# Optimization experiments

Measured on AMD Instinct MI355X. Metric: run time of the kernel, lower is better.

The kernel has to match this reference:

```python
import jax, jax.numpy as jnp
import numpy as np

R_ITER = 3
EPS = 1e-7  # keras.backend.epsilon()


def squash(v, axis=-1):
    s2 = jnp.sum(jnp.square(v), axis=axis, keepdims=True)
    scale = s2 / (1.0 + s2) / jnp.sqrt(s2 + EPS)
    return scale * v


def setup_inputs() -> dict:
    key = jax.random.key(0)
    kx, kw = jax.random.split(key)
    B, N_IN, D_IN = 64, 2048, 8
    N_OUT, D_OUT = 32, 16
    x = jax.random.normal(kx, (B, N_IN, D_IN), dtype=jnp.float32)
    # W matches keras weight (1, N_IN//shared, N_OUT, D_OUT, D_IN) with shared=1,
    # stored here without the leading broadcast dim. RandomNormal(stddev=0.1).
    W = 0.1 * jax.random.normal(kw, (N_IN, N_OUT, D_OUT, D_IN), dtype=jnp.float32)
    return {"x": x, "W": W}


def reference(x, W):
    # predictions u_hat[b, i, j, :] = W[i, j] @ x[b, i]  -> [B, N_in, N_out, D_out]
    preds = jnp.einsum('nodi,bni->bnod', W, x)
    N_in, N_out = preds.shape[1], preds.shape[2]
    # raw routing logits start at zeros with broadcast batch dim (as in TF code)
    raw = jnp.zeros((1, N_in, N_out), dtype=x.dtype)
    for i in range(R_ITER):
        rw = jax.nn.softmax(raw, axis=2)                      # softmax over output caps
        s = jnp.sum(rw[..., None] * preds, axis=1)            # [B, N_out, D_out]
        v = squash(s, axis=-1)                                # squash over capsule dim
        if i < R_ITER - 1:
            # agreement: <u_hat_ij, v_j>
            raw = raw + jnp.einsum('bnod,bod->bno', preds, v)
    return v, rw
```

## Files before the change

### kernel.cpp

```cpp
#include <hip/hip_runtime.h>

static constexpr int B_    = 64;
static constexpr int N_    = 2048;
static constexpr int DI_   = 8;
static constexpr int O_    = 32;
static constexpr int P_    = 16;
static constexpr int OP_   = O_ * P_;
static constexpr int M_    = OP_ * B_;
static constexpr int CHUNK_ = 8;
static constexpr int NBLK_  = N_ / CHUNK_;

template <int MODE, bool ATOMIC>
__global__ __launch_bounds__(1024, 4)
void fused_pass(const float* __restrict__ x, const float* __restrict__ W,
                const float* __restrict__ v_in, float* __restrict__ s_out,
                float* __restrict__ rw_out) {
  __shared__ float x_lds[CHUNK_ * 8 * 65];
  __shared__ float a_lds[2][O_ * B_];
  const int tid  = threadIdx.x;
  const int lane = tid & 63;
  const int wave = tid >> 6;
  const int n0   = blockIdx.x * CHUNK_;

  #pragma unroll
  for (int k = 0; k < 4; ++k) {
    int d = k * 1024 + tid;
    int b = d >> 6, rem = d & 63;
    x_lds[rem * 65 + b] = x[b * (N_ * DI_) + n0 * DI_ + rem];
  }

  float s_r[32];
  #pragma unroll
  for (int q = 0; q < 32; ++q) s_r[q] = 0.0f;

  __syncthreads();

  #pragma unroll 1
  for (int nn = 0; nn < CHUNK_; ++nn) {
    const int n = n0 + nn;
    float xr[8];
    #pragma unroll
    for (int i = 0; i < 8; ++i) xr[i] = x_lds[(nn * 8 + i) * 65 + lane];

    float pr[2][16];
    float ao0 = 0.0f, ao1 = 0.0f;

    #pragma unroll
    for (int oo = 0; oo < 2; ++oo) {
      const int o_u = __builtin_amdgcn_readfirstlane(wave * 2 + oo);
      const float* wp = W + (size_t)(n * O_ + o_u) * (P_ * DI_);

      float4 va0, va1, va2, va3;
      if (MODE != 0) {
        const float4* vp =
            (const float4*)(v_in + (size_t)lane * OP_ + (wave * 2 + oo) * P_);
        va0 = vp[0]; va1 = vp[1]; va2 = vp[2]; va3 = vp[3];
      }

      float acc = 0.0f;
      #pragma unroll
      for (int p = 0; p < P_; ++p) {
        float pv = wp[p * 8 + 0] * xr[0];
        pv = __builtin_fmaf(wp[p * 8 + 1], xr[1], pv);
        pv = __builtin_fmaf(wp[p * 8 + 2], xr[2], pv);
        pv = __builtin_fmaf(wp[p * 8 + 3], xr[3], pv);
        pv = __builtin_fmaf(wp[p * 8 + 4], xr[4], pv);
        pv = __builtin_fmaf(wp[p * 8 + 5], xr[5], pv);
        pv = __builtin_fmaf(wp[p * 8 + 6], xr[6], pv);
        pv = __builtin_fmaf(wp[p * 8 + 7], xr[7], pv);
        if (MODE == 0) {
          s_r[oo * 16 + p] += pv;
        } else {
          pr[oo][p] = pv;
          const float vc = (p < 4)  ? ((p & 3) == 0 ? va0.x : (p & 3) == 1 ? va0.y : (p & 3) == 2 ? va0.z : va0.w)
                         : (p < 8)  ? ((p & 3) == 0 ? va1.x : (p & 3) == 1 ? va1.y : (p & 3) == 2 ? va1.z : va1.w)
                         : (p < 12) ? ((p & 3) == 0 ? va2.x : (p & 3) == 1 ? va2.y : (p & 3) == 2 ? va2.z : va2.w)
                                    : ((p & 3) == 0 ? va3.x : (p & 3) == 1 ? va3.y : (p & 3) == 2 ? va3.z : va3.w);
          acc = __builtin_fmaf(pv, vc, acc);
        }
      }
      if (MODE != 0) {
        if (oo == 0) ao0 = acc; else ao1 = acc;
        a_lds[nn & 1][(wave * 2 + oo) * B_ + lane] = acc;
      }
    }

    if (MODE != 0) {
      __syncthreads();

      float Z = 0.0f;
      #pragma unroll
      for (int o = 0; o < O_; ++o) Z += __expf(a_lds[nn & 1][o * B_ + lane]);
      const float rZ  = 1.0f / Z;
      const float rw0 = __expf(ao0) * rZ;
      const float rw1 = __expf(ao1) * rZ;

      #pragma unroll
      for (int p = 0; p < P_; ++p) {
        s_r[p]      = __builtin_fmaf(rw0, pr[0][p], s_r[p]);
        s_r[16 + p] = __builtin_fmaf(rw1, pr[1][p], s_r[16 + p]);
      }
      if (MODE == 2) {
        float2 t; t.x = rw0; t.y = rw1;
        *(float2*)(rw_out + ((size_t)lane * N_ + n) * O_ + wave * 2) = t;
      }
    }
  }

  if (ATOMIC) {
    #pragma unroll
    for (int oo = 0; oo < 2; ++oo) {
      float* sp = s_out + (size_t)((wave * 2 + oo) * P_) * B_ + lane;
      #pragma unroll
      for (int p = 0; p < P_; ++p) atomicAdd(&sp[p * B_], s_r[oo * 16 + p]);
    }
  } else {
    #pragma unroll
    for (int oo = 0; oo < 2; ++oo) {
      float* sp = s_out + (size_t)blockIdx.x * M_ +
                  (size_t)((wave * 2 + oo) * P_) * B_ + lane;
      #pragma unroll
      for (int p = 0; p < P_; ++p) sp[p * B_] = s_r[oo * 16 + p];
    }
  }
}

__global__ __launch_bounds__(1024)
void reduce1(const float* __restrict__ spart, float* __restrict__ p2, int K) {
  const int g  = blockIdx.x >> 4;
  const int mc = blockIdx.x & 15;
  const int kpg = K >> 4;
  const int m0 = mc * 2048 + threadIdx.x;
  float a0 = 0.0f, a1 = 0.0f;
  const float* p = spart + (size_t)(g * kpg) * M_;
  for (int k = 0; k < kpg; ++k) {
    a0 += p[(size_t)k * M_ + m0];
    a1 += p[(size_t)k * M_ + m0 + 1024];
  }
  p2[(size_t)g * M_ + m0]        = a0;
  p2[(size_t)g * M_ + m0 + 1024] = a1;
}

__global__ __launch_bounds__(1024)
void v_kernel(const float* __restrict__ src, int ngroups, float scale,
              const float* __restrict__ v_add, float* __restrict__ v_out,
              float* __restrict__ zero_buf) {
  __shared__ float sq[P_ * 64];
  const int t = threadIdx.x;
  const int b = t & 63;
  const int p = t >> 6;
  const int o = blockIdx.x;
  const int q = o * P_ + p;
  float acc = 0.0f;
  for (int g = 0; g < ngroups; ++g) acc += src[(size_t)g * M_ + q * 64 + b];
  acc *= scale;
  sq[p * 64 + b] = acc * acc;
  if (zero_buf) zero_buf[blockIdx.x * 1024 + t] = 0.0f;
  __syncthreads();
  float s2 = 0.0f;
  #pragma unroll
  for (int pp = 0; pp < P_; ++pp) s2 += sq[pp * 64 + b];
  float sc = (s2 / (1.0f + s2)) / sqrtf(s2 + 1e-7f);
  float v = acc * sc;
  const int idx = b * OP_ + q;
  v_out[idx] = v + (v_add ? v_add[idx] : 0.0f);
}

extern "C" void kernel_launch(void* const* d_in, const int* in_sizes, int n_in,
                              void* d_out, int out_size, void* d_ws, size_t ws_size,
                              hipStream_t stream) {
  (void)in_sizes; (void)n_in; (void)out_size;
  const float* x = (const float*)d_in[0];
  const float* W = (const float*)d_in[1];
  float* out_v  = (float*)d_out;
  float* out_rw = out_v + (size_t)B_ * O_ * P_;
  float* vws   = (float*)d_ws;
  float* vsum  = vws + M_;
  float* p2    = vsum + M_;
  float* spart = p2 + 16 * M_;

  const size_t need = (size_t)(2 * M_ + 16 * M_ + (size_t)NBLK_ * M_) * 4;

  dim3 gF(NBLK_), bF(1024), gV(O_), bV(1024), gR(256);
  if (ws_size >= need) {
    fused_pass<0, false><<<gF, bF, 0, stream>>>(x, W, nullptr, spart, nullptr);
    reduce1<<<gR, bF, 0, stream>>>(spart, p2, NBLK_);
    v_kernel<<<gV, bV, 0, stream>>>(p2, 16, 1.0f / 32.0f, nullptr, vws, nullptr);
    fused_pass<1, false><<<gF, bF, 0, stream>>>(x, W, vws, spart, nullptr);
    reduce1<<<gR, bF, 0, stream>>>(spart, p2, NBLK_);
    v_kernel<<<gV, bV, 0, stream>>>(p2, 16, 1.0f, vws, vsum, nullptr);
    fused_pass<2, false><<<gF, bF, 0, stream>>>(x, W, vsum, spart, out_rw);
    reduce1<<<gR, bF, 0, stream>>>(spart, p2, NBLK_);
    v_kernel<<<gV, bV, 0, stream>>>(p2, 16, 1.0f, nullptr, out_v, nullptr);
  } else {
    float* sAb = p2;
    float* sBb = sAb + M_;
    hipMemsetAsync(sAb, 0, (size_t)M_ * sizeof(float), stream);
    fused_pass<0, true><<<gF, bF, 0, stream>>>(x, W, nullptr, sAb, nullptr);
    v_kernel<<<gV, bV, 0, stream>>>(sAb, 1, 1.0f / 32.0f, nullptr, vws, sBb);
    fused_pass<1, true><<<gF, bF, 0, stream>>>(x, W, vws, sBb, nullptr);
    v_kernel<<<gV, bV, 0, stream>>>(sBb, 1, 1.0f, vws, vsum, sAb);
    fused_pass<2, true><<<gF, bF, 0, stream>>>(x, W, vsum, sAb, out_rw);
    v_kernel<<<gV, bV, 0, stream>>>(sAb, 1, 1.0f, nullptr, out_v, nullptr);
  }
}
```

Measured before the change: 271.5 us.

## Double-buffer W slices into LDS via async global_load_lds and cut softmax exps

Each wave now streams its 1 KB portion of the next capsule's W slice straight into a double-buffered LDS array with global_load_lds, waiting on vmcnt before use. The FMA loop then reads W as float4 from LDS instead of issuing per-element global (scalar) loads. The v vectors are loaded once per block into registers rather than on every capsule. The softmax normaliser is built from per-wave partial sums of exponentials, so each thread does two expf plus 16 LDS adds instead of 32 expf. The larger LDS footprint may reduce how many blocks fit per CU, and the hand-written waitcnt relies on vmcnt ordering.

```diff
diff --git a/kernel.cpp b/kernel.cpp
--- a/kernel.cpp
+++ b/kernel.cpp
@@ -9,6 +9,14 @@
 static constexpr int M_    = OP_ * B_;
 static constexpr int CHUNK_ = 8;
 static constexpr int NBLK_  = N_ / CHUNK_;
+static constexpr int WSLICE_ = O_ * P_ * DI_;
+
+__device__ __forceinline__ void stage_w16(const float* g, float* l) {
+  __builtin_amdgcn_global_load_lds(
+      (const __attribute__((address_space(1))) void*)g,
+      (__attribute__((address_space(3))) void*)l,
+      16, 0, 0);
+}
 
 template <int MODE, bool ATOMIC>
 __global__ __launch_bounds__(1024, 4)
@@ -16,7 +24,8 @@
                 const float* __restrict__ v_in, float* __restrict__ s_out,
                 float* __restrict__ rw_out) {
   __shared__ float x_lds[CHUNK_ * 8 * 65];
-  __shared__ float a_lds[2][O_ * B_];
+  __shared__ __align__(16) float w_lds[2][WSLICE_];
+  __shared__ float z_lds[2][16 * B_];
   const int tid  = threadIdx.x;
   const int lane = tid & 63;
   const int wave = tid >> 6;
@@ -29,15 +38,41 @@
     x_lds[rem * 65 + b] = x[b * (N_ * DI_) + n0 * DI_ + rem];
   }
 
+  float va[2][16];
+  if (MODE != 0) {
+    #pragma unroll
+    for (int oo = 0; oo < 2; ++oo) {
+      const float4* vp =
+          (const float4*)(v_in + (size_t)lane * OP_ + (wave * 2 + oo) * P_);
+      const float4 t0 = vp[0], t1 = vp[1], t2 = vp[2], t3 = vp[3];
+      va[oo][0]  = t0.x; va[oo][1]  = t0.y; va[oo][2]  = t0.z; va[oo][3]  = t0.w;
+      va[oo][4]  = t1.x; va[oo][5]  = t1.y; va[oo][6]  = t1.z; va[oo][7]  = t1.w;
+      va[oo][8]  = t2.x; va[oo][9]  = t2.y; va[oo][10] = t2.z; va[oo][11] = t2.w;
+      va[oo][12] = t3.x; va[oo][13] = t3.y; va[oo][14] = t3.z; va[oo][15] = t3.w;
+    }
+  }
+
   float s_r[32];
   #pragma unroll
   for (int q = 0; q < 32; ++q) s_r[q] = 0.0f;
 
+  stage_w16(W + (size_t)n0 * WSLICE_ + wave * 256 + lane * 4,
+            &w_lds[0][wave * 256]);
+
   __syncthreads();
 
   #pragma unroll 1
   for (int nn = 0; nn < CHUNK_; ++nn) {
     const int n = n0 + nn;
+
+    if (nn + 1 < CHUNK_) {
+      stage_w16(W + (size_t)(n + 1) * WSLICE_ + wave * 256 + lane * 4,
+                &w_lds[(nn + 1) & 1][wave * 256]);
+      asm volatile("s_waitcnt vmcnt(1)" ::: "memory");
+    } else {
+      asm volatile("s_waitcnt vmcnt(0)" ::: "memory");
+    }
+
     float xr[8];
     #pragma unroll
     for (int i = 0; i < 8; ++i) xr[i] = x_lds[(nn * 8 + i) * 65 + lane];
@@ -47,53 +82,42 @@
 
     #pragma unroll
     for (int oo = 0; oo < 2; ++oo) {
-      const int o_u = __builtin_amdgcn_readfirstlane(wave * 2 + oo);
-      const float* wp = W + (size_t)(n * O_ + o_u) * (P_ * DI_);
-
-      float4 va0, va1, va2, va3;
-      if (MODE != 0) {
-        const float4* vp =
-            (const float4*)(v_in + (size_t)lane * OP_ + (wave * 2 + oo) * P_);
-        va0 = vp[0]; va1 = vp[1]; va2 = vp[2]; va3 = vp[3];
-      }
-
+      const float4* wl = (const float4*)&w_lds[nn & 1][(wave * 2 + oo) * 128];
       float acc = 0.0f;
       #pragma unroll
       for (int p = 0; p < P_; ++p) {
-        float pv = wp[p * 8 + 0] * xr[0];
-        pv = __builtin_fmaf(wp[p * 8 + 1], xr[1], pv);
-        pv = __builtin_fmaf(wp[p * 8 + 2], xr[2], pv);
-        pv = __builtin_fmaf(wp[p * 8 + 3], xr[3], pv);
-        pv = __builtin_fmaf(wp[p * 8 + 4], xr[4], pv);
-        pv = __builtin_fmaf(wp[p * 8 + 5], xr[5], pv);
-        pv = __builtin_fmaf(wp[p * 8 + 6], xr[6], pv);
-        pv = __builtin_fmaf(wp[p * 8 + 7], xr[7], pv);
+        const float4 w0 = wl[2 * p];
+        const float4 w1 = wl[2 * p + 1];
+        float pv = w0.x * xr[0];
+        pv = __builtin_fmaf(w0.y, xr[1], pv);
+        pv = __builtin_fmaf(w0.z, xr[2], pv);
+        pv = __builtin_fmaf(w0.w, xr[3], pv);
+        pv = __builtin_fmaf(w1.x, xr[4], pv);
+        pv = __builtin_fmaf(w1.y, xr[5], pv);
+        pv = __builtin_fmaf(w1.z, xr[6], pv);
+        pv = __builtin_fmaf(w1.w, xr[7], pv);
         if (MODE == 0) {
           s_r[oo * 16 + p] += pv;
         } else {
           pr[oo][p] = pv;
-          const float vc = (p < 4)  ? ((p & 3) == 0 ? va0.x : (p & 3) == 1 ? va0.y : (p & 3) == 2 ? va0.z : va0.w)
-                         : (p < 8)  ? ((p & 3) == 0 ? va1.x : (p & 3) == 1 ? va1.y : (p & 3) == 2 ? va1.z : va1.w)
-                         : (p < 12) ? ((p & 3) == 0 ? va2.x : (p & 3) == 1 ? va2.y : (p & 3) == 2 ? va2.z : va2.w)
-                                    : ((p & 3) == 0 ? va3.x : (p & 3) == 1 ? va3.y : (p & 3) == 2 ? va3.z : va3.w);
-          acc = __builtin_fmaf(pv, vc, acc);
+          acc = __builtin_fmaf(pv, va[oo][p], acc);
         }
       }
-      if (MODE != 0) {
-        if (oo == 0) ao0 = acc; else ao1 = acc;
-        a_lds[nn & 1][(wave * 2 + oo) * B_ + lane] = acc;
-      }
+      if (MODE != 0) { if (oo == 0) ao0 = acc; else ao1 = acc; }
     }
 
     if (MODE != 0) {
+      const float e0 = __expf(ao0);
+      const float e1 = __expf(ao1);
+      z_lds[nn & 1][wave * B_ + lane] = e0 + e1;
       __syncthreads();
 
       float Z = 0.0f;
       #pragma unroll
-      for (int o = 0; o < O_; ++o) Z += __expf(a_lds[nn & 1][o * B_ + lane]);
+      for (int w = 0; w < 16; ++w) Z += z_lds[nn & 1][w * B_ + lane];
       const float rZ  = 1.0f / Z;
-      const float rw0 = __expf(ao0) * rZ;
-      const float rw1 = __expf(ao1) * rZ;
+      const float rw0 = e0 * rZ;
+      const float rw1 = e1 * rZ;
 
       #pragma unroll
       for (int p = 0; p < P_; ++p) {
```

Result: faster. 229.6 us (-15.4%).

## Remap fused pass to stage W slices in LDS and reduce softmax with DPP

Applied to the files above, without the earlier changes.

The fused routing pass now assigns lanes to (output capsule, half of pose vector) and waves to batch groups of four. Each W slice for the next input capsule is double-buffered into LDS with global_load_lds using an XOR swizzle, and x values are broadcast through readfirstlane. The per-row softmax over output capsules becomes a DPP/shuffle reduction instead of an LDS exchange plus barrier, and partial sums are written as float4 in b-major layout. The v_kernel is adjusted to that layout. This is meant to cut redundant global W reads and scattered stores, at the cost of a barrier per step and more register pressure.

```diff
diff --git a/kernel.cpp b/kernel.cpp
--- a/kernel.cpp
+++ b/kernel.cpp
@@ -9,118 +9,160 @@
 static constexpr int M_    = OP_ * B_;
 static constexpr int CHUNK_ = 8;
 static constexpr int NBLK_  = N_ / CHUNK_;
+static constexpr int WSLICE_ = O_ * P_ * DI_;
+
+__device__ __forceinline__ void stage_w16(const float* g, float* l) {
+  __builtin_amdgcn_global_load_lds(
+      (const __attribute__((address_space(1))) void*)g,
+      (__attribute__((address_space(3))) void*)l,
+      16, 0, 0);
+}
+
+template <int CTRL>
+__device__ __forceinline__ float dpp_add(float v) {
+  int t = __builtin_amdgcn_update_dpp(0, __float_as_int(v), CTRL, 0xf, 0xf, false);
+  return v + __int_as_float(t);
+}
+
+__device__ __forceinline__ float rfl(float v) {
+  return __int_as_float(__builtin_amdgcn_readfirstlane(__float_as_int(v)));
+}
 
 template <int MODE, bool ATOMIC>
 __global__ __launch_bounds__(1024, 4)
 void fused_pass(const float* __restrict__ x, const float* __restrict__ W,
                 const float* __restrict__ v_in, float* __restrict__ s_out,
                 float* __restrict__ rw_out) {
-  __shared__ float x_lds[CHUNK_ * 8 * 65];
-  __shared__ float a_lds[2][O_ * B_];
+  __shared__ __align__(16) float w_lds[2][WSLICE_];
+  __shared__ __align__(16) float x_lds[CHUNK_ * 512];
   const int tid  = threadIdx.x;
   const int lane = tid & 63;
   const int wave = tid >> 6;
+  const int wu   = __builtin_amdgcn_readfirstlane(wave);
+  const int o    = lane >> 1;
+  const int ph   = lane & 1;
+  const int q3   = o & 7;
   const int n0   = blockIdx.x * CHUNK_;
 
+  {
+    const int bs = tid >> 4;
+    const int cs = tid & 15;
+    const float4 xv =
+        *(const float4*)(x + (size_t)bs * (N_ * DI_) + n0 * DI_ + cs * 4);
+    *(float4*)&x_lds[(cs >> 1) * 512 + bs * 8 + (cs & 1) * 4] = xv;
+  }
+
+  float vv[4][8];
+  if (MODE != 0) {
+    #pragma unroll
+    for (int bb = 0; bb < 4; ++bb) {
+      const float4* vp = (const float4*)(v_in + (size_t)(wu * 4 + bb) * OP_ +
+                                         o * P_ + ph * 8);
+      const float4 a = vp[0], c = vp[1];
+      vv[bb][0] = a.x; vv[bb][1] = a.y; vv[bb][2] = a.z; vv[bb][3] = a.w;
+      vv[bb][4] = c.x; vv[bb][5] = c.y; vv[bb][6] = c.z; vv[bb][7] = c.w;
+    }
+  }
+
+  float s_r[4][8];
   #pragma unroll
-  for (int k = 0; k < 4; ++k) {
-    int d = k * 1024 + tid;
-    int b = d >> 6, rem = d & 63;
-    x_lds[rem * 65 + b] = x[b * (N_ * DI_) + n0 * DI_ + rem];
-  }
-
-  float s_r[32];
-  #pragma unroll
-  for (int q = 0; q < 32; ++q) s_r[q] = 0.0f;
-
-  __syncthreads();
+  for (int bb = 0; bb < 4; ++bb)
+    #pragma unroll
+    for (int pp = 0; pp < 8; ++pp) s_r[bb][pp] = 0.0f;
+
+  const int sg = tid ^ ((tid >> 5) & 7);
+
+  stage_w16(W + (size_t)n0 * WSLICE_ + (size_t)sg * 4, &w_lds[0][wu * 256]);
 
   #pragma unroll 1
   for (int nn = 0; nn < CHUNK_; ++nn) {
-    const int n = n0 + nn;
-    float xr[8];
-    #pragma unroll
-    for (int i = 0; i < 8; ++i) xr[i] = x_lds[(nn * 8 + i) * 65 + lane];
-
-    float pr[2][16];
-    float ao0 = 0.0f, ao1 = 0.0f;
-
-    #pragma unroll
-    for (int oo = 0; oo < 2; ++oo) {
-      const int o_u = __builtin_amdgcn_readfirstlane(wave * 2 + oo);
-      const float* wp = W + (size_t)(n * O_ + o_u) * (P_ * DI_);
-
-      float4 va0, va1, va2, va3;
-      if (MODE != 0) {
-        const float4* vp =
-            (const float4*)(v_in + (size_t)lane * OP_ + (wave * 2 + oo) * P_);
-        va0 = vp[0]; va1 = vp[1]; va2 = vp[2]; va3 = vp[3];
-      }
-
-      float acc = 0.0f;
+    asm volatile("s_waitcnt vmcnt(0)" ::: "memory");
+    __syncthreads();
+    if (nn + 1 < CHUNK_)
+      stage_w16(W + (size_t)(n0 + nn + 1) * WSLICE_ + (size_t)sg * 4,
+                &w_lds[(nn + 1) & 1][wu * 256]);
+
+    float xs[4][8];
+    #pragma unroll
+    for (int bb = 0; bb < 4; ++bb) {
+      const float4 xa = *(const float4*)&x_lds[nn * 512 + (wu * 4 + bb) * 8];
+      const float4 xc = *(const float4*)&x_lds[nn * 512 + (wu * 4 + bb) * 8 + 4];
+      xs[bb][0] = rfl(xa.x); xs[bb][1] = rfl(xa.y);
+      xs[bb][2] = rfl(xa.z); xs[bb][3] = rfl(xa.w);
+      xs[bb][4] = rfl(xc.x); xs[bb][5] = rfl(xc.y);
+      xs[bb][6] = rfl(xc.z); xs[bb][7] = rfl(xc.w);
+    }
+
+    float pr[4][8];
+    float acc[4] = {0.0f, 0.0f, 0.0f, 0.0f};
+    const int wbase = ((nn & 1) ? WSLICE_ : 0) + o * 128 + ph * 64;
+
+    #pragma unroll
+    for (int pp = 0; pp < 8; ++pp) {
+      const int c0 = (2 * pp) ^ q3;
+      const int c1 = (2 * pp + 1) ^ q3;
+      const float4 w0 = *(const float4*)&w_lds[0][wbase + c0 * 4];
+      const float4 w1 = *(const float4*)&w_lds[0][wbase + c1 * 4];
       #pragma unroll
-      for (int p = 0; p < P_; ++p) {
-        float pv = wp[p * 8 + 0] * xr[0];
-        pv = __builtin_fmaf(wp[p * 8 + 1], xr[1], pv);
-        pv = __builtin_fmaf(wp[p * 8 + 2], xr[2], pv);
-        pv = __builtin_fmaf(wp[p * 8 + 3], xr[3], pv);
-        pv = __builtin_fmaf(wp[p * 8 + 4], xr[4], pv);
-        pv = __builtin_fmaf(wp[p * 8 + 5], xr[5], pv);
-        pv = __builtin_fmaf(wp[p * 8 + 6], xr[6], pv);
-        pv = __builtin_fmaf(wp[p * 8 + 7], xr[7], pv);
+      for (int bb = 0; bb < 4; ++bb) {
+        float pv = w0.x * xs[bb][0];
+        pv = __builtin_fmaf(w0.y, xs[bb][1], pv);
+        pv = __builtin_fmaf(w0.z, xs[bb][2], pv);
+        pv = __builtin_fmaf(w0.w, xs[bb][3], pv);
+        pv = __builtin_fmaf(w1.x, xs[bb][4], pv);
+        pv = __builtin_fmaf(w1.y, xs[bb][5], pv);
+        pv = __builtin_fmaf(w1.z, xs[bb][6], pv);
+        pv = __builtin_fmaf(w1.w, xs[bb][7], pv);
         if (MODE == 0) {
-          s_r[oo * 16 + p] += pv;
+          s_r[bb][pp] += pv;
         } else {
-          pr[oo][p] = pv;
-          const float vc = (p < 4)  ? ((p & 3) == 0 ? va0.x : (p & 3) == 1 ? va0.y : (p & 3) == 2 ? va0.z : va0.w)
-                         : (p < 8)  ? ((p & 3) == 0 ? va1.x : (p & 3) == 1 ? va1.y : (p & 3) == 2 ? va1.z : va1.w)
-                         : (p < 12) ? ((p & 3) == 0 ? va2.x : (p & 3) == 1 ? va2.y : (p & 3) == 2 ? va2.z : va2.w)
-                                    : ((p & 3) == 0 ? va3.x : (p & 3) == 1 ? va3.y : (p & 3) == 2 ? va3.z : va3.w);
-          acc = __builtin_fmaf(pv, vc, acc);
+          pr[bb][pp] = pv;
+          acc[bb] = __builtin_fmaf(pv, vv[bb][pp], acc[bb]);
         }
       }
-      if (MODE != 0) {
-        if (oo == 0) ao0 = acc; else ao1 = acc;
-        a_lds[nn & 1][(wave * 2 + oo) * B_ + lane] = acc;
+    }
+
+    if (MODE != 0) {
+      #pragma unroll
+      for (int bb = 0; bb < 4; ++bb) {
+        const float full = dpp_add<0xB1>(acc[bb]);
+        const float e = __expf(full);
+        float srow = e;
+        srow = dpp_add<0x121>(srow);
+        srow = dpp_add<0x122>(srow);
+        srow = dpp_add<0x124>(srow);
+        srow = dpp_add<0x128>(srow);
+        float t2 = srow + __shfl_xor(srow, 16);
+        const float S = t2 + __shfl_xor(t2, 32);
+        const float rw = (2.0f * e) / S;
+        #pragma unroll
+        for (int pp = 0; pp < 8; ++pp)
+          s_r[bb][pp] = __builtin_fmaf(rw, pr[bb][pp], s_r[bb][pp]);
+        if (MODE == 2) {
+          if (ph == 0)
+            rw_out[((size_t)(wu * 4 + bb) * N_ + (n0 + nn)) * O_ + o] = rw;
+        }
       }
     }
-
-    if (MODE != 0) {
-      __syncthreads();
-
-      float Z = 0.0f;
+  }
+
+  if (ATOMIC) {
+    #pragma unroll
+    for (int bb = 0; bb < 4; ++bb) {
+      float* sp = s_out + (size_t)(wu * 4 + bb) * OP_ + o * P_ + ph * 8;
       #pragma unroll
-      for (int o = 0; o < O_; ++o) Z += __expf(a_lds[nn & 1][o * B_ + lane]);
-      const float rZ  = 1.0f / Z;
-      const float rw0 = __expf(ao0) * rZ;
-      const float rw1 = __expf(ao1) * rZ;
-
-      #pragma unroll
-      for (int p = 0; p < P_; ++p) {
-        s_r[p]      = __builtin_fmaf(rw0, pr[0][p], s_r[p]);
-        s_r[16 + p] = __builtin_fmaf(rw1, pr[1][p], s_r[16 + p]);
-      }
-      if (MODE == 2) {
-        float2 t; t.x = rw0; t.y = rw1;
-        *(float2*)(rw_out + ((size_t)lane * N_ + n) * O_ + wave * 2) = t;
-      }
-    }
-  }
-
-  if (ATOMIC) {
-    #pragma unroll
-    for (int oo = 0; oo < 2; ++oo) {
-      float* sp = s_out + (size_t)((wave * 2 + oo) * P_) * B_ + lane;
-      #pragma unroll
-      for (int p = 0; p < P_; ++p) atomicAdd(&sp[p * B_], s_r[oo * 16 + p]);
+      for (int pp = 0; pp < 8; ++pp) atomicAdd(&sp[pp], s_r[bb][pp]);
     }
   } else {
     #pragma unroll
-    for (int oo = 0; oo < 2; ++oo) {
+    for (int bb = 0; bb < 4; ++bb) {
       float* sp = s_out + (size_t)blockIdx.x * M_ +
-                  (size_t)((wave * 2 + oo) * P_) * B_ + lane;
-      #pragma unroll
-      for (int p = 0; p < P_; ++p) sp[p * B_] = s_r[oo * 16 + p];
+                  (size_t)(wu * 4 + bb) * OP_ + o * P_ + ph * 8;
+      float4 st0, st1;
+      st0.x = s_r[bb][0]; st0.y = s_r[bb][1]; st0.z = s_r[bb][2]; st0.w = s_r[bb][3];
+      st1.x = s_r[bb][4]; st1.y = s_r[bb][5]; st1.z = s_r[bb][6]; st1.w = s_r[bb][7];
+      *(float4*)sp = st0;
+      *(float4*)(sp + 4) = st1;
     }
   }
 }
@@ -145,21 +187,22 @@
 void v_kernel(const float* __restrict__ src, int ngroups, float scale,
               const float* __restrict__ v_add, float* __restrict__ v_out,
               float* __restrict__ zero_buf) {
-  __shared__ float sq[P_ * 64];
+  __shared__ float sq[P_ * 65];
   const int t = threadIdx.x;
-  const int b = t & 63;
-  const int p = t >> 6;
+  const int p = t & 15;
+  const int b = t >> 4;
   const int o = blockIdx.x;
   const int q = o * P_ + p;
   float acc = 0.0f;
-  for (int g = 0; g < ngroups; ++g) acc += src[(size_t)g * M_ + q * 64 + b];
+  for (int g = 0; g < ngroups; ++g)
+    acc += src[(size_t)g * M_ + (size_t)b * OP_ + q];
   acc *= scale;
-  sq[p * 64 + b] = acc * acc;
+  sq[p * 65 + b] = acc * acc;
   if (zero_buf) zero_buf[blockIdx.x * 1024 + t] = 0.0f;
   __syncthreads();
   float s2 = 0.0f;
   #pragma unroll
-  for (int pp = 0; pp < P_; ++pp) s2 += sq[pp * 64 + b];
+  for (int pp = 0; pp < P_; ++pp) s2 += sq[pp * 65 + b];
   float sc = (s2 / (1.0f + s2)) / sqrtf(s2 + 1e-7f);
   float v = acc * sc;
   const int idx = b * OP_ + q;
```

After: 272.4 us. Within noise of the previous version (+0.4%).

## Compute capsule predictions with split-bf16 MFMA and batch-split blocks

Applied to the files above, without the earlier changes.

Replaces the scalar FP32 FMA prediction loop with 16x16x32 bf16 MFMA instructions, using a hi/lo bf16 split (three MFMAs) to approximate FP32 precision. Each block now covers half the batch with 512 threads, and agreement dot-products are reduced with cross-lane shuffles. The s-partial layout changes to batch-major, written through an LDS transpose epilogue, and v_kernel is remapped to match. The MFMA uses only K=8 of its 32 slots and the split conversion adds ALU work, so the gain over FP32 FMA depends on the kernel being compute-bound rather than memory-bound.

```diff
diff --git a/kernel.cpp b/kernel.cpp
--- a/kernel.cpp
+++ b/kernel.cpp
@@ -1,4 +1,7 @@
 #include <hip/hip_runtime.h>
+
+typedef __attribute__((ext_vector_type(4))) float f32x4;
+typedef __attribute__((ext_vector_type(8))) short bf16x8;
 
 static constexpr int B_    = 64;
 static constexpr int N_    = 2048;
@@ -10,117 +13,167 @@
 static constexpr int CHUNK_ = 8;
 static constexpr int NBLK_  = N_ / CHUNK_;
 
+__device__ __forceinline__ int rfl_i(int v) {
+  return __builtin_amdgcn_readfirstlane(v);
+}
+
+__device__ __forceinline__ void cvt_hilo(f32x4 a, f32x4 b, bf16x8& hi, bf16x8& lo) {
+  uint32_t u0 = __float_as_uint(a[0]), u1 = __float_as_uint(a[1]);
+  uint32_t u2 = __float_as_uint(a[2]), u3 = __float_as_uint(a[3]);
+  uint32_t u4 = __float_as_uint(b[0]), u5 = __float_as_uint(b[1]);
+  uint32_t u6 = __float_as_uint(b[2]), u7 = __float_as_uint(b[3]);
+  union { uint32_t u[4]; bf16x8 v; } H, L;
+  H.u[0] = (u0 >> 16) | (u1 & 0xFFFF0000u);
+  H.u[1] = (u2 >> 16) | (u3 & 0xFFFF0000u);
+  H.u[2] = (u4 >> 16) | (u5 & 0xFFFF0000u);
+  H.u[3] = (u6 >> 16) | (u7 & 0xFFFF0000u);
+  float l0 = a[0] - __uint_as_float(u0 & 0xFFFF0000u);
+  float l1 = a[1] - __uint_as_float(u1 & 0xFFFF0000u);
+  float l2 = a[2] - __uint_as_float(u2 & 0xFFFF0000u);
+  float l3 = a[3] - __uint_as_float(u3 & 0xFFFF0000u);
+  float l4 = b[0] - __uint_as_float(u4 & 0xFFFF0000u);
+  float l5 = b[1] - __uint_as_float(u5 & 0xFFFF0000u);
+  float l6 = b[2] - __uint_as_float(u6 & 0xFFFF0000u);
+  float l7 = b[3] - __uint_as_float(u7 & 0xFFFF0000u);
+  L.u[0] = (__float_as_uint(l0) >> 16) | (__float_as_uint(l1) & 0xFFFF0000u);
+  L.u[1] = (__float_as_uint(l2) >> 16) | (__float_as_uint(l3) & 0xFFFF0000u);
+  L.u[2] = (__float_as_uint(l4) >> 16) | (__float_as_uint(l5) & 0xFFFF0000u);
+  L.u[3] = (__float_as_uint(l6) >> 16) | (__float_as_uint(l7) & 0xFFFF0000u);
+  hi = H.v;
+  lo = L.v;
+}
+
+#define MFMA16(a, b, c) __builtin_amdgcn_mfma_f32_16x16x32_bf16((a), (b), (c), 0, 0, 0)
+
 template <int MODE, bool ATOMIC>
-__global__ __launch_bounds__(1024, 4)
+__global__ __launch_bounds__(512, 2)
 void fused_pass(const float* __restrict__ x, const float* __restrict__ W,
                 const float* __restrict__ v_in, float* __restrict__ s_out,
                 float* __restrict__ rw_out) {
-  __shared__ float x_lds[CHUNK_ * 8 * 65];
-  __shared__ float a_lds[2][O_ * B_];
+  __shared__ __align__(16) float x_lds[32 * 64];
+  __shared__ __align__(16) float z_lds[2][32][4];
+  __shared__ __align__(16) float epi[8][256];
   const int tid  = threadIdx.x;
   const int lane = tid & 63;
-  const int wave = tid >> 6;
-  const int n0   = blockIdx.x * CHUNK_;
-
+  const int wu   = rfl_i(tid >> 6);
+  const int qg   = wu >> 1;
+  const int bt   = wu & 1;
+  const int lb   = lane & 15;
+  const int kq   = lane >> 4;
+  const int cn   = blockIdx.x >> 1;
+  const int bh   = blockIdx.x & 1;
+  const int n0   = cn * CHUNK_;
+  const int bcol = bh * 32 + bt * 16 + lb;
+
+  {
+    const int bl = tid >> 4;
+    const int ch = tid & 15;
+    *(f32x4*)&x_lds[bl * 64 + ch * 4] = *(const f32x4*)(
+        x + (size_t)(bh * 32 + bl) * (N_ * DI_) + n0 * DI_ + ch * 4);
+  }
+  __syncthreads();
+
+  f32x4 s_f[8];
   #pragma unroll
-  for (int k = 0; k < 4; ++k) {
-    int d = k * 1024 + tid;
-    int b = d >> 6, rem = d & 63;
-    x_lds[rem * 65 + b] = x[b * (N_ * DI_) + n0 * DI_ + rem];
-  }
-
-  float s_r[32];
-  #pragma unroll
-  for (int q = 0; q < 32; ++q) s_r[q] = 0.0f;
-
-  __syncthreads();
+  for (int t = 0; t < 8; ++t) s_f[t] = (f32x4){0.f, 0.f, 0.f, 0.f};
+
+  bf16x8 z8 = {0, 0, 0, 0, 0, 0, 0, 0};
+  bf16x8 Ahi = z8, Alo = z8, Bhi = z8, Blo = z8;
 
   #pragma unroll 1
   for (int nn = 0; nn < CHUNK_; ++nn) {
     const int n = n0 + nn;
-    float xr[8];
+
+    if (lane < 16) {
+      f32x4 xa = *(const f32x4*)&x_lds[(bt * 16 + lane) * 64 + nn * 8];
+      f32x4 xb = *(const f32x4*)&x_lds[(bt * 16 + lane) * 64 + nn * 8 + 4];
+      cvt_hilo(xa, xb, Bhi, Blo);
+    }
+
+    f32x4 pr_f[8];
+    float ef[8];
+    float zacc = 0.0f;
+
     #pragma unroll
-    for (int i = 0; i < 8; ++i) xr[i] = x_lds[(nn * 8 + i) * 65 + lane];
-
-    float pr[2][16];
-    float ao0 = 0.0f, ao1 = 0.0f;
-
+    for (int t = 0; t < 8; ++t) {
+      const int o = qg * 8 + t;
+      if (lane < 16) {
+        const float* wp = W + ((size_t)n * 512 + o * 16 + lane) * 8;
+        f32x4 wa = *(const f32x4*)wp;
+        f32x4 wb = *(const f32x4*)(wp + 4);
+        cvt_hilo(wa, wb, Ahi, Alo);
+      }
+      if (MODE == 0) {
+        s_f[t] = MFMA16(Alo, Bhi, s_f[t]);
+        s_f[t] = MFMA16(Ahi, Blo, s_f[t]);
+        s_f[t] = MFMA16(Ahi, Bhi, s_f[t]);
+      } else {
+        f32x4 d = (f32x4){0.f, 0.f, 0.f, 0.f};
+        d = MFMA16(Alo, Bhi, d);
+        d = MFMA16(Ahi, Blo, d);
+        d = MFMA16(Ahi, Bhi, d);
+        pr_f[t] = d;
+        f32x4 vt = *(const f32x4*)(v_in + (size_t)bcol * OP_ + o * 16 + kq * 4);
+        float dd = d[0] * vt[0];
+        dd = __builtin_fmaf(d[1], vt[1], dd);
+        dd = __builtin_fmaf(d[2], vt[2], dd);
+        dd = __builtin_fmaf(d[3], vt[3], dd);
+        dd += __shfl_xor(dd, 16);
+        dd += __shfl_xor(dd, 32);
+        ef[t] = __expf(dd);
+        zacc += ef[t];
+      }
+    }
+
+    if (MODE != 0) {
+      if (lane < 16) z_lds[nn & 1][bt * 16 + lane][qg] = zacc;
+      __syncthreads();
+      f32x4 zv = *(const f32x4*)&z_lds[nn & 1][bt * 16 + lb][0];
+      const float rZ = 1.0f / (zv[0] + zv[1] + zv[2] + zv[3]);
+      #pragma unroll
+      for (int t = 0; t < 8; ++t) {
+        const float rw = ef[t] * rZ;
+        s_f[t][0] = __builtin_fmaf(rw, pr_f[t][0], s_f[t][0]);
+        s_f[t][1] = __builtin_fmaf(rw, pr_f[t][1], s_f[t][1]);
+        s_f[t][2] = __builtin_fmaf(rw, pr_f[t][2], s_f[t][2]);
+        s_f[t][3] = __builtin_fmaf(rw, pr_f[t][3], s_f[t][3]);
+      }
+      if (MODE == 2) {
+        if (lane < 16) {
+          f32x4 r0, r1;
+          r0[0] = ef[0] * rZ; r0[1] = ef[1] * rZ;
+          r0[2] = ef[2] * rZ; r0[3] = ef[3] * rZ;
+          r1[0] = ef[4] * rZ; r1[1] = ef[5] * rZ;
+          r1[2] = ef[6] * rZ; r1[3] = ef[7] * rZ;
+          float* rp = rw_out + ((size_t)bcol * N_ + n) * O_ + qg * 8;
+          *(f32x4*)rp = r0;
+          *(f32x4*)(rp + 4) = r1;
+        }
+      }
+    }
+  }
+
+  {
+    float* ep = &epi[wu][0];
     #pragma unroll
-    for (int oo = 0; oo < 2; ++oo) {
-      const int o_u = __builtin_amdgcn_readfirstlane(wave * 2 + oo);
-      const float* wp = W + (size_t)(n * O_ + o_u) * (P_ * DI_);
-
-      float4 va0, va1, va2, va3;
-      if (MODE != 0) {
-        const float4* vp =
-            (const float4*)(v_in + (size_t)lane * OP_ + (wave * 2 + oo) * P_);
-        va0 = vp[0]; va1 = vp[1]; va2 = vp[2]; va3 = vp[3];
-      }
-
-      float acc = 0.0f;
-      #pragma unroll
-      for (int p = 0; p < P_; ++p) {
-        float pv = wp[p * 8 + 0] * xr[0];
-        pv = __builtin_fmaf(wp[p * 8 + 1], xr[1], pv);
-        pv = __builtin_fmaf(wp[p * 8 + 2], xr[2], pv);
-        pv = __builtin_fmaf(wp[p * 8 + 3], xr[3], pv);
-        pv = __builtin_fmaf(wp[p * 8 + 4], xr[4], pv);
-        pv = __builtin_fmaf(wp[p * 8 + 5], xr[5], pv);
-        pv = __builtin_fmaf(wp[p * 8 + 6], xr[6], pv);
-        pv = __builtin_fmaf(wp[p * 8 + 7], xr[7], pv);
-        if (MODE == 0) {
-          s_r[oo * 16 + p] += pv;
-        } else {
-          pr[oo][p] = pv;
-          const float vc = (p < 4)  ? ((p & 3) == 0 ? va0.x : (p & 3) == 1 ? va0.y : (p & 3) == 2 ? va0.z : va0.w)
-                         : (p < 8)  ? ((p & 3) == 0 ? va1.x : (p & 3) == 1 ? va1.y : (p & 3) == 2 ? va1.z : va1.w)
-                         : (p < 12) ? ((p & 3) == 0 ? va2.x : (p & 3) == 1 ? va2.y : (p & 3) == 2 ? va2.z : va2.w)
-                                    : ((p & 3) == 0 ? va3.x : (p & 3) == 1 ? va3.y : (p & 3) == 2 ? va3.z : va3.w);
-          acc = __builtin_fmaf(pv, vc, acc);
-        }
-      }
-      if (MODE != 0) {
-        if (oo == 0) ao0 = acc; else ao1 = acc;
-        a_lds[nn & 1][(wave * 2 + oo) * B_ + lane] = acc;
-      }
-    }
-
-    if (MODE != 0) {
-      __syncthreads();
-
-      float Z = 0.0f;
-      #pragma unroll
-      for (int o = 0; o < O_; ++o) Z += __expf(a_lds[nn & 1][o * B_ + lane]);
-      const float rZ  = 1.0f / Z;
-      const float rw0 = __expf(ao0) * rZ;
-      const float rw1 = __expf(ao1) * rZ;
-
-      #pragma unroll
-      for (int p = 0; p < P_; ++p) {
-        s_r[p]      = __builtin_fmaf(rw0, pr[0][p], s_r[p]);
-        s_r[16 + p] = __builtin_fmaf(rw1, pr[1][p], s_r[16 + p]);
-      }
-      if (MODE == 2) {
-        float2 t; t.x = rw0; t.y = rw1;
-        *(float2*)(rw_out + ((size_t)lane * N_ + n) * O_ + wave * 2) = t;
-      }
-    }
-  }
-
-  if (ATOMIC) {
-    #pragma unroll
-    for (int oo = 0; oo < 2; ++oo) {
-      float* sp = s_out + (size_t)((wave * 2 + oo) * P_) * B_ + lane;
-      #pragma unroll
-      for (int p = 0; p < P_; ++p) atomicAdd(&sp[p * B_], s_r[oo * 16 + p]);
-    }
-  } else {
-    #pragma unroll
-    for (int oo = 0; oo < 2; ++oo) {
-      float* sp = s_out + (size_t)blockIdx.x * M_ +
-                  (size_t)((wave * 2 + oo) * P_) * B_ + lane;
-      #pragma unroll
-      for (int p = 0; p < P_; ++p) sp[p * B_] = s_r[oo * 16 + p];
+    for (int t = 0; t < 8; ++t) {
+      const int o = qg * 8 + t;
+      *(f32x4*)&ep[lane * 4] = s_f[t];
+      asm volatile("s_waitcnt lgkmcnt(0)" ::: "memory");
+      __builtin_amdgcn_sched_barrier(0);
+      f32x4 rv = *(const f32x4*)&ep[((lane & 3) * 16 + (lane >> 2)) * 4];
+      asm volatile("s_waitcnt lgkmcnt(0)" ::: "memory");
+      __builtin_amdgcn_sched_barrier(0);
+      const size_t qoff =
+          (size_t)(bh * 32 + bt * 16 + (lane >> 2)) * OP_ + o * 16 + (lane & 3) * 4;
+      if (ATOMIC) {
+        atomicAdd(&s_out[qoff + 0], rv[0]);
+        atomicAdd(&s_out[qoff + 1], rv[1]);
+        atomicAdd(&s_out[qoff + 2], rv[2]);
+        atomicAdd(&s_out[qoff + 3], rv[3]);
+      } else {
+        *(f32x4*)(s_out + (size_t)cn * M_ + qoff) = rv;
+      }
     }
   }
 }
@@ -145,24 +198,25 @@
 void v_kernel(const float* __restrict__ src, int ngroups, float scale,
               const float* __restrict__ v_add, float* __restrict__ v_out,
               float* __restrict__ zero_buf) {
-  __shared__ float sq[P_ * 64];
+  __shared__ float sq[P_ * 65];
   const int t = threadIdx.x;
-  const int b = t & 63;
-  const int p = t >> 6;
+  const int p = t & 15;
+  const int b = t >> 4;
   const int o = blockIdx.x;
   const int q = o * P_ + p;
+  const int idx = b * OP_ + q;
   float acc = 0.0f;
-  for (int g = 0; g < ngroups; ++g) acc += src[(size_t)g * M_ + q * 64 + b];
+  for (int g = 0; g < ngroups; ++g)
+    acc += src[(size_t)g * M_ + idx];
   acc *= scale;
-  sq[p * 64 + b] = acc * acc;
+  sq[p * 65 + b] = acc * acc;
   if (zero_buf) zero_buf[blockIdx.x * 1024 + t] = 0.0f;
   __syncthreads();
   float s2 = 0.0f;
   #pragma unroll
-  for (int pp = 0; pp < P_; ++pp) s2 += sq[pp * 64 + b];
+  for (int pp = 0; pp < P_; ++pp) s2 += sq[pp * 65 + b];
   float sc = (s2 / (1.0f + s2)) / sqrtf(s2 + 1e-7f);
   float v = acc * sc;
-  const int idx = b * OP_ + q;
   v_out[idx] = v + (v_add ? v_add[idx] : 0.0f);
 }
 
@@ -181,16 +235,16 @@
 
   const size_t need = (size_t)(2 * M_ + 16 * M_ + (size_t)NBLK_ * M_) * 4;
 
-  dim3 gF(NBLK_), bF(1024), gV(O_), bV(1024), gR(256);
+  dim3 gF(2 * NBLK_), bF(512), gV(O_), bV(1024), gR(256), bR(1024);
   if (ws_size >= need) {
     fused_pass<0, false><<<gF, bF, 0, stream>>>(x, W, nullptr, spart, nullptr);
-    reduce1<<<gR, bF, 0, stream>>>(spart, p2, NBLK_);
+    reduce1<<<gR, bR, 0, stream>>>(spart, p2, NBLK_);
     v_kernel<<<gV, bV, 0, stream>>>(p2, 16, 1.0f / 32.0f, nullptr, vws, nullptr);
     fused_pass<1, false><<<gF, bF, 0, stream>>>(x, W, vws, spart, nullptr);
-    reduce1<<<gR, bF, 0, stream>>>(spart, p2, NBLK_);
+    reduce1<<<gR, bR, 0, stream>>>(spart, p2, NBLK_);
     v_kernel<<<gV, bV, 0, stream>>>(p2, 16, 1.0f, vws, vsum, nullptr);
     fused_pass<2, false><<<gF, bF, 0, stream>>>(x, W, vsum, spart, out_rw);
-    reduce1<<<gR, bF, 0, stream>>>(spart, p2, NBLK_);
+    reduce1<<<gR, bR, 0, stream>>>(spart, p2, NBLK_);
     v_kernel<<<gV, bV, 0, stream>>>(p2, 16, 1.0f, nullptr, out_v, nullptr);
   } else {
     float* sAb = p2;
```

After: 306.8 us. +13.0%, slower.
